# Performance work log

Hardware: AMD Instinct MI355X
Metric: run time of the kernel (lower is better)

The kernel has to match this reference:

```python
import jax, jax.numpy as jnp
import numpy as np

EMBED_DIM = 1024
NUM_HEADS = 16
HEAD_DIM = EMBED_DIM // NUM_HEADS
B, S = 2, 2048


def setup_inputs() -> dict:
    key = jax.random.key(0)
    ks = jax.random.split(key, 11)
    f32 = jnp.float32
    return {
        "q": jax.random.normal(ks[0], (B, S, EMBED_DIM), f32),
        "k": jax.random.normal(ks[1], (B, S, EMBED_DIM), f32),
        "v": jax.random.normal(ks[2], (B, S, EMBED_DIM), f32),
        # per-head projection weights stacked over heads: [H, E, Dh]
        "Wq": jax.random.normal(ks[3], (NUM_HEADS, EMBED_DIM, HEAD_DIM), f32),
        "Wk": jax.random.normal(ks[4], (NUM_HEADS, EMBED_DIM, HEAD_DIM), f32),
        "Wv": jax.random.normal(ks[5], (NUM_HEADS, EMBED_DIM, HEAD_DIM), f32),
        "bq": jax.random.normal(ks[6], (NUM_HEADS, HEAD_DIM), f32),
        "bk": jax.random.normal(ks[7], (NUM_HEADS, HEAD_DIM), f32),
        "bv": jax.random.normal(ks[8], (NUM_HEADS, HEAD_DIM), f32),
        "Wo": jax.random.normal(ks[9], (EMBED_DIM, EMBED_DIM), f32),
        "bo": jax.random.normal(ks[10], (EMBED_DIM,), f32),
    }


def reference(q, k, v, Wq, Wk, Wv, bq, bk, bv, Wo, bo):
    scale = jnp.asarray(np.sqrt(HEAD_DIM), q.dtype)
    # batched per-head projections: [B,S,E] x [H,E,D] -> [B,H,S,D]
    Q = jnp.einsum("bse,hed->bhsd", q, Wq) + bq[None, :, None, :]
    K = jnp.einsum("bse,hed->bhsd", k, Wk) + bk[None, :, None, :]
    V = jnp.einsum("bse,hed->bhsd", v, Wv) + bv[None, :, None, :]
    # attention scores [B,H,S,S]; original applies mask to a discarded tensor,
    # so output is unmasked softmax(QK^T/scale) @ V
    att = jnp.einsum("bhsd,bhtd->bhst", Q, K) / scale
    att = jax.nn.softmax(att, axis=-1)
    ctx = jnp.einsum("bhst,bhtd->bhsd", att, V)  # [B,H,S,D]
    # concat heads (head order preserved) then output projection
    ctx = ctx.transpose(0, 2, 1, 3).reshape(ctx.shape[0], ctx.shape[2], -1)  # [B,S,E]
    return ctx @ Wo + bo
```

## Files before the change

kernel.cpp:

```cpp
#include <hip/hip_runtime.h>
#include <hip/hip_bf16.h>

typedef unsigned short u16;
typedef unsigned int   u32;
typedef _Float16 f16;
typedef __attribute__((ext_vector_type(4))) float f32x4;
typedef __attribute__((ext_vector_type(8))) short s16x8;
typedef __attribute__((ext_vector_type(8))) f16 f16x8;
typedef __attribute__((ext_vector_type(2))) __fp16 fp16x2;
typedef __attribute__((ext_vector_type(4))) u16 u16x4;
typedef __attribute__((ext_vector_type(2))) u32 u32x2;

#define DI __device__ __forceinline__

static constexpr int Bb = 2, Ss = 2048, Hh = 16, Dd = 64, Ee = 1024;
static constexpr int Mrows = Bb * Ss;
static constexpr size_t NE = (size_t)Mrows * Ee;
static constexpr size_t WN = (size_t)Ee * Ee;
static constexpr float QSCALE = 0.125f * 1.44269504088896f;

DI float bf2f(u16 h) { u32 u = ((u32)h) << 16; return __builtin_bit_cast(float, u); }
DI u16 f2bf(float f) {
    u32 u = __builtin_bit_cast(u32, f);
    u32 r = (u + 0x7FFFu + ((u >> 16) & 1u)) >> 16;
    return (u16)r;
}
DI u16 f2h(float f) { f16 h = (f16)f; return __builtin_bit_cast(u16, h); }
DI u32 pkrtz(float a, float b) {
    fp16x2 r = __builtin_amdgcn_cvt_pkrtz(a, b);
    return __builtin_bit_cast(u32, r);
}
DI float ex2(float x) { return __builtin_amdgcn_exp2f(x); }

#define MFMA_BF(a, b, c) __builtin_amdgcn_mfma_f32_16x16x32_bf16((a), (b), (c), 0, 0, 0)
#define MFMA_F16(a, b, c) __builtin_amdgcn_mfma_f32_16x16x32_f16( \
    __builtin_bit_cast(f16x8, (a)), __builtin_bit_cast(f16x8, (b)), (c), 0, 0, 0)

DI void gld16(const u16* g, u16* l) {
    __builtin_amdgcn_global_load_lds((const __attribute__((address_space(1))) void*)g,
                                     (__attribute__((address_space(3))) void*)l, 16, 0, 0);
}

__global__ __launch_bounds__(256) void k_split3(
    const float* __restrict__ q, const float* __restrict__ k, const float* __restrict__ v,
    u16* __restrict__ qh, u16* __restrict__ ql,
    u16* __restrict__ kh, u16* __restrict__ kl, u16* __restrict__ vh) {
    int i = blockIdx.x * 256 + threadIdx.x;
    int y = blockIdx.y;
    if (y == 2) { vh[i] = f2h(v[i]); return; }
    const float* s = y ? k : q;
    u16* h = y ? kh : qh;
    u16* l = y ? kl : ql;
    float val = s[i];
    u16 hh = f2bf(val);
    h[i] = hh;
    l[i] = f2bf(val - bf2f(hh));
}

__global__ __launch_bounds__(256) void k_wprep(
    const float* __restrict__ Wq, const float* __restrict__ Wk,
    const float* __restrict__ Wv, const float* __restrict__ Wo,
    u16* __restrict__ WqTh, u16* __restrict__ WqTl,
    u16* __restrict__ WkTh, u16* __restrict__ WkTl,
    u16* __restrict__ WvT, u16* __restrict__ WoT) {
    __shared__ float Ts[64 * 65];
    const int y = blockIdx.y;
    const int ti = blockIdx.x >> 4, tj = blockIdx.x & 15;
    const float* W = (y == 0) ? Wq : (y == 1) ? Wk : (y == 2) ? Wv : Wo;
    const int t = threadIdx.x;
    const int col = t & 63, rb = (t >> 6) * 16;
#pragma unroll
    for (int rr = 0; rr < 16; rr++) {
        int row = rb + rr;
        float v = (y < 3) ? W[(size_t)ti * 65536 + (size_t)(tj * 64 + row) * 64 + col]
                          : W[(size_t)(tj * 64 + row) * Ee + ti * 64 + col];
        Ts[row * 65 + col] = v;
    }
    __syncthreads();
#pragma unroll
    for (int rr = 0; rr < 16; rr++) {
        int orow = rb + rr;
        int ocol = col;
        float v = Ts[ocol * 65 + orow];
        size_t oidx = (size_t)(ti * 64 + orow) * Ee + tj * 64 + ocol;
        if (y == 0) {
            u16 hh = f2bf(v); WqTh[oidx] = hh; WqTl[oidx] = f2bf(v - bf2f(hh));
        } else if (y == 1) {
            u16 hh = f2bf(v); WkTh[oidx] = hh; WkTl[oidx] = f2bf(v - bf2f(hh));
        } else if (y == 2) {
            WvT[oidx] = f2h(v);
        } else {
            WoT[oidx] = f2h(v);
        }
    }
}

template <int SPLIT, int F16, int OUTMODE>
DI void gemm_body(const u16* __restrict__ Ah, const u16* __restrict__ Al,
                  const u16* __restrict__ Bh, const u16* __restrict__ Bl,
                  const float* __restrict__ bias,
                  u16* __restrict__ C16h, u16* __restrict__ C16l, float* __restrict__ Cf,
                  float scale, u16* As0, u16* As1, u16* Bs0, u16* Bs1) {
    constexpr int M = Mrows, N = Ee, K = Ee;
    const int tid = threadIdx.x;
    const int wave = tid >> 6, lane = tid & 63;
    const int quad = lane >> 4, l16 = lane & 15;
    const int m0 = blockIdx.y * 128, n0 = blockIdx.x * 128;
    const int wm = (wave >> 1) * 64, wn = (wave & 1) * 64;

    f32x4 acc[4][4];
#pragma unroll
    for (int i = 0; i < 4; i++)
#pragma unroll
        for (int j = 0; j < 4; j++) acc[i][j] = (f32x4)0.0f;

    for (int kk = 0; kk < K; kk += 32) {
        __syncthreads();
#pragma unroll
        for (int i = 0; i < 2; i++) {
            int c = tid + i * 256;
            int row = c >> 2, j = c & 3;
            size_t ga = (size_t)(m0 + row) * K + kk + j * 8;
            gld16(Ah + ga, As0 + c * 8);
            if constexpr (SPLIT) gld16(Al + ga, As1 + c * 8);
            size_t gb = (size_t)(n0 + row) * K + kk + j * 8;
            gld16(Bh + gb, Bs0 + c * 8);
            if constexpr (SPLIT) gld16(Bl + gb, Bs1 + c * 8);
        }
        __syncthreads();

        s16x8 bf[4][2];
#pragma unroll
        for (int nt = 0; nt < 4; nt++) {
            int r = wn + nt * 16 + l16;
            bf[nt][0] = *(const s16x8*)&Bs0[r * 32 + quad * 8];
            if constexpr (SPLIT) bf[nt][1] = *(const s16x8*)&Bs1[r * 32 + quad * 8];
        }
#pragma unroll
        for (int mt = 0; mt < 4; mt++) {
            int r = wm + mt * 16 + l16;
            s16x8 a0 = *(const s16x8*)&As0[r * 32 + quad * 8];
            s16x8 a1;
            if constexpr (SPLIT) a1 = *(const s16x8*)&As1[r * 32 + quad * 8];
#pragma unroll
            for (int nt = 0; nt < 4; nt++) {
                if constexpr (F16) {
                    acc[mt][nt] = MFMA_F16(a0, bf[nt][0], acc[mt][nt]);
                } else {
                    acc[mt][nt] = MFMA_BF(a0, bf[nt][0], acc[mt][nt]);
                    if constexpr (SPLIT) {
                        acc[mt][nt] = MFMA_BF(a0, bf[nt][1], acc[mt][nt]);
                        acc[mt][nt] = MFMA_BF(a1, bf[nt][0], acc[mt][nt]);
                    }
                }
            }
        }
    }

#pragma unroll
    for (int mt = 0; mt < 4; mt++)
#pragma unroll
        for (int nt = 0; nt < 4; nt++) {
            int gn = n0 + wn + nt * 16 + l16;
            float bs = bias[gn];
            if constexpr (OUTMODE == 1) {
                int gm = m0 + wm + mt * 16 + quad * 4;
                u16x4 pk;
#pragma unroll
                for (int r = 0; r < 4; r++) pk[r] = f2h((acc[mt][nt][r] + bs) * scale);
                *(u16x4*)&C16h[(size_t)gn * M + gm] = pk;
            } else {
#pragma unroll
                for (int r = 0; r < 4; r++) {
                    int gm = m0 + wm + mt * 16 + quad * 4 + r;
                    float v = (acc[mt][nt][r] + bs) * scale;
                    if constexpr (OUTMODE == 0) {
                        Cf[(size_t)gm * N + gn] = v;
                    } else {
                        u16 hh = f2bf(v);
                        C16h[(size_t)gm * N + gn] = hh;
                        C16l[(size_t)gm * N + gn] = f2bf(v - bf2f(hh));
                    }
                }
            }
        }
}

__global__ __launch_bounds__(256, 3) void k_qkv(
    const u16* __restrict__ qh, const u16* __restrict__ ql,
    const u16* __restrict__ kh, const u16* __restrict__ kl,
    const u16* __restrict__ vh,
    const u16* __restrict__ WqTh, const u16* __restrict__ WqTl,
    const u16* __restrict__ WkTh, const u16* __restrict__ WkTl,
    const u16* __restrict__ WvT,
    const float* __restrict__ bq, const float* __restrict__ bk, const float* __restrict__ bv,
    u16* __restrict__ Qh, u16* __restrict__ Ql2,
    u16* __restrict__ Kh, u16* __restrict__ Kl2, u16* __restrict__ Vt) {
    __shared__ u16 As[2][128 * 32];
    __shared__ u16 Bs[2][128 * 32];
    int z = blockIdx.z;
    if (z == 0)
        gemm_body<1, 0, 2>(qh, ql, WqTh, WqTl, bq, Qh, Ql2, nullptr, QSCALE,
                           As[0], As[1], Bs[0], Bs[1]);
    else if (z == 1)
        gemm_body<1, 0, 2>(kh, kl, WkTh, WkTl, bk, Kh, Kl2, nullptr, 1.0f,
                           As[0], As[1], Bs[0], Bs[1]);
    else
        gemm_body<0, 1, 1>(vh, nullptr, WvT, nullptr, bv, Vt, nullptr, nullptr, 1.0f,
                           As[0], As[1], Bs[0], Bs[1]);
}

__global__ __launch_bounds__(256, 3) void k_out(
    const u16* __restrict__ ctx, const u16* __restrict__ WoT,
    const float* __restrict__ bo, float* __restrict__ out) {
    __shared__ u16 As[128 * 32];
    __shared__ u16 Bs[128 * 32];
    gemm_body<0, 1, 0>(ctx, nullptr, WoT, nullptr, bo, nullptr, nullptr, out, 1.0f,
                       As, nullptr, Bs, nullptr);
}

__global__ __launch_bounds__(256, 2) void k_attn(
    const u16* __restrict__ Qh, const u16* __restrict__ Ql,
    const u16* __restrict__ Kh, const u16* __restrict__ Kl,
    const u16* __restrict__ Vt, u16* __restrict__ ctx) {
    const int bh = blockIdx.x;
    const int b = bh >> 4, h = bh & 15;
    const int q0 = blockIdx.y * 128;
    const int rowBase = b * Ss + q0;
    const int hc = h * 64;

    __shared__ u16 Ks[2][64 * 64];
    __shared__ u16 Vs[64 * 64];
    __shared__ u16 Pw[4][32 * 72];

    const int tid = threadIdx.x;
    const int wave = tid >> 6, lane = tid & 63;
    const int quad = lane >> 4, l16 = lane & 15;

    const int c0 = tid, c1 = tid + 256;
    const int srow0 = c0 >> 3, sgj0 = c0 & 7;
    const int srow1 = c1 >> 3, sgj1 = c1 & 7;
    const int soff0 = srow0 * 64 + (sgj0 ^ (srow0 & 7)) * 8;
    const int soff1 = srow1 * 64 + (sgj1 ^ (srow1 & 7)) * 8;

    s16x8 rkh0, rkh1, rkl0, rkl1, rv0, rv1;
    auto loadT = [&](int t0) {
        const int kRowBase = b * Ss + t0;
        rkh0 = *(const s16x8*)(Kh + (size_t)(kRowBase + srow0) * Ee + hc + sgj0 * 8);
        rkl0 = *(const s16x8*)(Kl + (size_t)(kRowBase + srow0) * Ee + hc + sgj0 * 8);
        rv0  = *(const s16x8*)(Vt + (size_t)(hc + srow0) * Mrows + kRowBase + sgj0 * 8);
        rkh1 = *(const s16x8*)(Kh + (size_t)(kRowBase + srow1) * Ee + hc + sgj1 * 8);
        rkl1 = *(const s16x8*)(Kl + (size_t)(kRowBase + srow1) * Ee + hc + sgj1 * 8);
        rv1  = *(const s16x8*)(Vt + (size_t)(hc + srow1) * Mrows + kRowBase + sgj1 * 8);
    };
    auto storeT = [&]() {
        *(s16x8*)&Ks[0][soff0] = rkh0;
        *(s16x8*)&Ks[0][soff1] = rkh1;
        *(s16x8*)&Ks[1][soff0] = rkl0;
        *(s16x8*)&Ks[1][soff1] = rkl1;
        *(s16x8*)&Vs[soff0] = rv0;
        *(s16x8*)&Vs[soff1] = rv1;
    };

    const int sw0 = ((0 * 4 + quad) ^ (l16 & 7)) * 8;
    const int sw1 = ((1 * 4 + quad) ^ (l16 & 7)) * 8;
    const u16* akb0 = &Ks[0][l16 * 64 + sw0];
    const u16* akb1 = &Ks[0][l16 * 64 + sw1];
    const u16* avb0 = &Vs[l16 * 64 + sw0];
    const u16* avb1 = &Vs[l16 * 64 + sw1];
    u16* pwb = &Pw[wave][l16 * 72 + quad * 4];
    const u16* pbb = &Pw[wave][l16 * 72 + quad * 8];

    s16x8 bq[2][2][2];
#pragma unroll
    for (int nt = 0; nt < 2; nt++) {
        int row = rowBase + wave * 32 + nt * 16 + l16;
#pragma unroll
        for (int kc = 0; kc < 2; kc++) {
            bq[nt][kc][0] = *(const s16x8*)(Qh + (size_t)row * Ee + hc + kc * 32 + quad * 8);
            bq[nt][kc][1] = *(const s16x8*)(Ql + (size_t)row * Ee + hc + kc * 32 + quad * 8);
        }
    }

    f32x4 o[2][4];
#pragma unroll
    for (int nt = 0; nt < 2; nt++)
#pragma unroll
        for (int dg = 0; dg < 4; dg++) o[nt][dg] = (f32x4)0.0f;
    float m_[2] = {-1e30f, -1e30f};
    float l_[2] = {0.f, 0.f};

    loadT(0);
    storeT();
    __syncthreads();

    for (int t0 = 0; t0 < Ss; t0 += 64) {
        const bool more = (t0 + 64) < Ss;
        if (more) loadT(t0 + 64);

        f32x4 st[2][4];
#pragma unroll
        for (int nt = 0; nt < 2; nt++)
#pragma unroll
            for (int mt = 0; mt < 4; mt++) st[nt][mt] = (f32x4)0.0f;
        __builtin_amdgcn_s_setprio(1);
#pragma unroll
        for (int mt = 0; mt < 4; mt++) {
            s16x8 akh0 = *(const s16x8*)(akb0 + mt * 1024);
            s16x8 akl0 = *(const s16x8*)(akb0 + mt * 1024 + 4096);
            s16x8 akh1 = *(const s16x8*)(akb1 + mt * 1024);
            s16x8 akl1 = *(const s16x8*)(akb1 + mt * 1024 + 4096);
#pragma unroll
            for (int nt = 0; nt < 2; nt++) {
                st[nt][mt] = MFMA_BF(akh0, bq[nt][0][0], st[nt][mt]);
                st[nt][mt] = MFMA_BF(akh0, bq[nt][0][1], st[nt][mt]);
                st[nt][mt] = MFMA_BF(akl0, bq[nt][0][0], st[nt][mt]);
                st[nt][mt] = MFMA_BF(akh1, bq[nt][1][0], st[nt][mt]);
                st[nt][mt] = MFMA_BF(akh1, bq[nt][1][1], st[nt][mt]);
                st[nt][mt] = MFMA_BF(akl1, bq[nt][1][0], st[nt][mt]);
            }
        }
        __builtin_amdgcn_s_setprio(0);

#pragma unroll
        for (int nt = 0; nt < 2; nt++) {
            float t01 = fmaxf(fmaxf(st[nt][0][0], st[nt][0][1]), fmaxf(st[nt][0][2], st[nt][0][3]));
            float t23 = fmaxf(fmaxf(st[nt][1][0], st[nt][1][1]), fmaxf(st[nt][1][2], st[nt][1][3]));
            float t45 = fmaxf(fmaxf(st[nt][2][0], st[nt][2][1]), fmaxf(st[nt][2][2], st[nt][2][3]));
            float t67 = fmaxf(fmaxf(st[nt][3][0], st[nt][3][1]), fmaxf(st[nt][3][2], st[nt][3][3]));
            float tmax = fmaxf(fmaxf(t01, t23), fmaxf(t45, t67));
            tmax = fmaxf(tmax, __shfl_xor(tmax, 16));
            tmax = fmaxf(tmax, __shfl_xor(tmax, 32));
            float mnew = fmaxf(m_[nt], tmax);
            float al = ex2(m_[nt] - mnew);
            m_[nt] = mnew;
            float psum = 0.f;
#pragma unroll
            for (int mt = 0; mt < 4; mt++) {
                float p0 = ex2(st[nt][mt][0] - mnew);
                float p1 = ex2(st[nt][mt][1] - mnew);
                float p2 = ex2(st[nt][mt][2] - mnew);
                float p3 = ex2(st[nt][mt][3] - mnew);
                psum += (p0 + p1) + (p2 + p3);
                u32x2 pk;
                pk[0] = pkrtz(p0, p1);
                pk[1] = pkrtz(p2, p3);
                *(u32x2*)(pwb + nt * 1152 + mt * 16) = pk;
            }
            psum += __shfl_xor(psum, 16);
            psum += __shfl_xor(psum, 32);
            l_[nt] = l_[nt] * al + psum;
#pragma unroll
            for (int dg = 0; dg < 4; dg++) o[nt][dg] *= al;
        }

        __builtin_amdgcn_s_setprio(1);
#pragma unroll
        for (int kc = 0; kc < 2; kc++) {
            s16x8 bp[2];
#pragma unroll
            for (int nt = 0; nt < 2; nt++)
                bp[nt] = *(const s16x8*)(pbb + nt * 1152 + kc * 32);
            const u16* avb = kc ? avb1 : avb0;
#pragma unroll
            for (int dg = 0; dg < 4; dg++) {
                s16x8 av = *(const s16x8*)(avb + dg * 1024);
#pragma unroll
                for (int nt = 0; nt < 2; nt++) o[nt][dg] = MFMA_F16(av, bp[nt], o[nt][dg]);
            }
        }
        __builtin_amdgcn_s_setprio(0);

        if (more) {
            __syncthreads();
            storeT();
            __syncthreads();
        }
    }

#pragma unroll
    for (int nt = 0; nt < 2; nt++) {
        float inv = 1.0f / l_[nt];
        int gm = rowBase + wave * 32 + nt * 16 + l16;
#pragma unroll
        for (int dg = 0; dg < 4; dg++) {
            u32x2 pk;
            pk[0] = pkrtz(o[nt][dg][0] * inv, o[nt][dg][1] * inv);
            pk[1] = pkrtz(o[nt][dg][2] * inv, o[nt][dg][3] * inv);
            *(u32x2*)&ctx[(size_t)gm * Ee + hc + dg * 16 + quad * 4] = pk;
        }
    }
}

extern "C" void kernel_launch(void* const* d_in, const int* in_sizes, int n_in,
                              void* d_out, int out_size, void* d_ws, size_t ws_size,
                              hipStream_t stream) {
    const float* q   = (const float*)d_in[0];
    const float* kin = (const float*)d_in[1];
    const float* v   = (const float*)d_in[2];
    const float* Wq  = (const float*)d_in[3];
    const float* Wk  = (const float*)d_in[4];
    const float* Wv  = (const float*)d_in[5];
    const float* bq  = (const float*)d_in[6];
    const float* bk  = (const float*)d_in[7];
    const float* bv  = (const float*)d_in[8];
    const float* Wo  = (const float*)d_in[9];
    const float* bo  = (const float*)d_in[10];

    u16* ws = (u16*)d_ws;
    u16 *qh = ws,          *ql = ws + NE,     *kh = ws + 2 * NE, *kl = ws + 3 * NE;
    u16 *vh = ws + 4 * NE;
    u16 *Qh = ws + 5 * NE, *Ql = ws + 6 * NE, *Kh = ws + 7 * NE, *Kl = ws + 8 * NE;
    u16 *Vt = ws + 9 * NE, *ctx = ws + 10 * NE;
    u16 *WqTh = ws + 11 * NE;
    u16 *WqTl = WqTh + WN, *WkTh = WqTh + 2 * WN, *WkTl = WqTh + 3 * WN;
    u16 *WvT = WqTh + 4 * WN, *WoT = WqTh + 5 * WN;

    dim3 b256(256);
    k_split3<<<dim3(NE / 256, 3), b256, 0, stream>>>(q, kin, v, qh, ql, kh, kl, vh);
    k_wprep<<<dim3(256, 4), b256, 0, stream>>>(Wq, Wk, Wv, Wo,
                                               WqTh, WqTl, WkTh, WkTl, WvT, WoT);

    k_qkv<<<dim3(8, 32, 3), b256, 0, stream>>>(qh, ql, kh, kl, vh,
                                               WqTh, WqTl, WkTh, WkTl, WvT,
                                               bq, bk, bv, Qh, Ql, Kh, Kl, Vt);

    k_attn<<<dim3(Bb * Hh, Ss / 128), b256, 0, stream>>>(Qh, Ql, Kh, Kl, Vt, ctx);

    k_out<<<dim3(8, 32), b256, 0, stream>>>(ctx, WoT, bo, (float*)d_out);
}
```

Measured before the change: 307.3 us.

## Double-buffer K/V tiles in LDS and drop one barrier per attention step

The attention kernel now keeps two LDS buffers for the K hi/lo and V tiles. Each iteration computes on one buffer while writing the next tile, already held in registers, into the other. The next global prefetch is issued right after that store, so global loads get a full iteration to land. This cuts the per-iteration barriers from two to one, at the cost of more LDS per block (roughly 66KB), which could limit occupancy.

```diff
diff --git a/kernel.cpp b/kernel.cpp
--- a/kernel.cpp
+++ b/kernel.cpp
@@ -229,8 +229,8 @@
     const int rowBase = b * Ss + q0;
     const int hc = h * 64;
 
-    __shared__ u16 Ks[2][64 * 64];
-    __shared__ u16 Vs[64 * 64];
+    __shared__ u16 Ks[2][2][64 * 64];
+    __shared__ u16 Vs[2][64 * 64];
     __shared__ u16 Pw[4][32 * 72];
 
     const int tid = threadIdx.x;
@@ -253,21 +253,21 @@
         rkl1 = *(const s16x8*)(Kl + (size_t)(kRowBase + srow1) * Ee + hc + sgj1 * 8);
         rv1  = *(const s16x8*)(Vt + (size_t)(hc + srow1) * Mrows + kRowBase + sgj1 * 8);
     };
-    auto storeT = [&]() {
-        *(s16x8*)&Ks[0][soff0] = rkh0;
-        *(s16x8*)&Ks[0][soff1] = rkh1;
-        *(s16x8*)&Ks[1][soff0] = rkl0;
-        *(s16x8*)&Ks[1][soff1] = rkl1;
-        *(s16x8*)&Vs[soff0] = rv0;
-        *(s16x8*)&Vs[soff1] = rv1;
+    auto storeT = [&](int bf) {
+        u16* Kd = &Ks[bf][0][0];
+        u16* Vd = &Vs[bf][0];
+        *(s16x8*)&Kd[soff0] = rkh0;
+        *(s16x8*)&Kd[soff1] = rkh1;
+        *(s16x8*)&Kd[4096 + soff0] = rkl0;
+        *(s16x8*)&Kd[4096 + soff1] = rkl1;
+        *(s16x8*)&Vd[soff0] = rv0;
+        *(s16x8*)&Vd[soff1] = rv1;
     };
 
     const int sw0 = ((0 * 4 + quad) ^ (l16 & 7)) * 8;
     const int sw1 = ((1 * 4 + quad) ^ (l16 & 7)) * 8;
-    const u16* akb0 = &Ks[0][l16 * 64 + sw0];
-    const u16* akb1 = &Ks[0][l16 * 64 + sw1];
-    const u16* avb0 = &Vs[l16 * 64 + sw0];
-    const u16* avb1 = &Vs[l16 * 64 + sw1];
+    const int kro0 = l16 * 64 + sw0;
+    const int kro1 = l16 * 64 + sw1;
     u16* pwb = &Pw[wave][l16 * 72 + quad * 4];
     const u16* pbb = &Pw[wave][l16 * 72 + quad * 8];
 
@@ -291,12 +291,14 @@
     float l_[2] = {0.f, 0.f};
 
     loadT(0);
-    storeT();
+    storeT(0);
+    loadT(64);
     __syncthreads();
 
     for (int t0 = 0; t0 < Ss; t0 += 64) {
-        const bool more = (t0 + 64) < Ss;
-        if (more) loadT(t0 + 64);
+        const int p = (t0 >> 6) & 1;
+        const u16* Kp = &Ks[p][0][0];
+        const u16* Vp = &Vs[p][0];
 
         f32x4 st[2][4];
 #pragma unroll
@@ -306,10 +308,10 @@
         __builtin_amdgcn_s_setprio(1);
 #pragma unroll
         for (int mt = 0; mt < 4; mt++) {
-            s16x8 akh0 = *(const s16x8*)(akb0 + mt * 1024);
-            s16x8 akl0 = *(const s16x8*)(akb0 + mt * 1024 + 4096);
-            s16x8 akh1 = *(const s16x8*)(akb1 + mt * 1024);
-            s16x8 akl1 = *(const s16x8*)(akb1 + mt * 1024 + 4096);
+            s16x8 akh0 = *(const s16x8*)(Kp + kro0 + mt * 1024);
+            s16x8 akl0 = *(const s16x8*)(Kp + kro0 + mt * 1024 + 4096);
+            s16x8 akh1 = *(const s16x8*)(Kp + kro1 + mt * 1024);
+            s16x8 akl1 = *(const s16x8*)(Kp + kro1 + mt * 1024 + 4096);
 #pragma unroll
             for (int nt = 0; nt < 2; nt++) {
                 st[nt][mt] = MFMA_BF(akh0, bq[nt][0][0], st[nt][mt]);
@@ -361,21 +363,21 @@
 #pragma unroll
             for (int nt = 0; nt < 2; nt++)
                 bp[nt] = *(const s16x8*)(pbb + nt * 1152 + kc * 32);
-            const u16* avb = kc ? avb1 : avb0;
+            const int vro = kc ? kro1 : kro0;
 #pragma unroll
             for (int dg = 0; dg < 4; dg++) {
-                s16x8 av = *(const s16x8*)(avb + dg * 1024);
+                s16x8 av = *(const s16x8*)(Vp + vro + dg * 1024);
 #pragma unroll
                 for (int nt = 0; nt < 2; nt++) o[nt][dg] = MFMA_F16(av, bp[nt], o[nt][dg]);
             }
         }
         __builtin_amdgcn_s_setprio(0);
 
-        if (more) {
-            __syncthreads();
-            storeT();
-            __syncthreads();
-        }
+        if (t0 + 64 < Ss) {
+            storeT(p ^ 1);
+            if (t0 + 128 < Ss) loadT(t0 + 128);
+        }
+        __syncthreads();
     }
 
 #pragma unroll
```

Result: no change. 304.8 us (-0.8%).
